# Optimization experiments

Hardware: AMD Instinct MI355X
Metric: run time of the kernel (lower is better)

Reference implementation:

```python
import jax, jax.numpy as jnp
import numpy as np

N = 4096        # nodes
E = 131072      # edges (avg degree 32)
IN_F = 256      # in_features
OUT_F = 64      # out_features per head
H = 8           # num_heads


def setup_inputs() -> dict:
    key = jax.random.key(0)
    k1, k2, k3, k4 = jax.random.split(key, 4)
    x = jax.random.normal(k1, (N, IN_F), dtype=jnp.float32)
    # xavier-ish scales for the learned params
    W = jax.random.normal(k2, (IN_F, OUT_F * H), dtype=jnp.float32) * 0.06
    a = jax.random.normal(k3, (2 * OUT_F, 1), dtype=jnp.float32) * 0.12
    edge_index = jax.random.randint(k4, (2, E), 0, N, dtype=jnp.int32)
    return {"x": x, "W": W, "a": a, "edge_index": edge_index}


def reference(x, W, a, edge_index):
    n = x.shape[0]
    Wh = (x @ W).reshape(n, H, OUT_F)          # [N, H, F]
    src, dst = edge_index[0], edge_index[1]
    # edge score: cat(Wh[src], Wh[dst]) @ a == Wh[src]@a1 + Wh[dst]@a2
    a1 = a[:OUT_F, 0]                           # [F]
    a2 = a[OUT_F:2 * OUT_F, 0]                  # [F]
    alpha_src = Wh @ a1                         # [N, H]
    alpha_dst = Wh @ a2                         # [N, H]
    edge_e = jax.nn.leaky_relu(alpha_src[src] + alpha_dst[dst], 0.2)  # [E, H]
    # dense scatter exactly as the original module (non-edges stay 0 in softmax)
    attention = jnp.zeros((n, n, H), dtype=x.dtype).at[src, dst].set(edge_e)
    attention = jax.nn.softmax(attention, axis=1)
    # dropout is identity in eval mode
    h_prime = jnp.einsum('nmh,mhf->nhf', attention, Wh)  # [N, H, F]
    return h_prime.reshape(n, H * OUT_F)        # concat=True
```

## Files before the change

### kernel.cpp

```cpp
#include <hip/hip_runtime.h>
#include <hip/hip_bf16.h>

constexpr int NN    = 4096;
constexpr int EE    = 131072;
constexpr int IN_F  = 256;
constexpr int OUT_F = 64;
constexpr int HH    = 8;
constexpr int HF    = OUT_F * HH;
constexpr int CAP   = 128;

typedef __attribute__((ext_vector_type(8))) short bf16x8;
typedef __attribute__((ext_vector_type(4))) float f32x4;

__device__ __forceinline__ unsigned short f2b(float f) {
    unsigned int u = __float_as_uint(f);
    u = u + 0x7FFFu + ((u >> 16) & 1u);
    return (unsigned short)(u >> 16);
}
__device__ __forceinline__ float b2f(unsigned int lo16) {
    return __uint_as_float(lo16 << 16);
}

__global__ __launch_bounds__(256) void prep(const float* __restrict__ W,
                                            unsigned short* __restrict__ WThi,
                                            unsigned short* __restrict__ WTlo,
                                            float* __restrict__ S,
                                            int* __restrict__ cnt) {
    int b = blockIdx.x, t = threadIdx.x;
    if (b < 64) {
        int n  = b * 8 + (t >> 5);
        int kb = (t & 31) * 8;
        unsigned short hi[8], lo[8];
#pragma unroll
        for (int j = 0; j < 8; ++j) {
            float f = W[(size_t)(kb + j) * HF + n];
            hi[j] = f2b(f);
            lo[j] = f2b(f - b2f(hi[j]));
        }
        size_t o = (size_t)n * 256 + kb;
        *(ushort4*)(WThi + o)     = make_ushort4(hi[0], hi[1], hi[2], hi[3]);
        *(ushort4*)(WThi + o + 4) = make_ushort4(hi[4], hi[5], hi[6], hi[7]);
        *(ushort4*)(WTlo + o)     = make_ushort4(lo[0], lo[1], lo[2], lo[3]);
        *(ushort4*)(WTlo + o + 4) = make_ushort4(lo[4], lo[5], lo[6], lo[7]);
    } else {
        int gt = (b - 64) * 256 + t;
        if (gt < NN) cnt[gt] = 0;
        else if (gt < NN + HF) S[gt - NN] = 0.f;
    }
}

__global__ __launch_bounds__(256) void gemm_mfma(const float* __restrict__ xf,
                                                 const unsigned short* __restrict__ WThi,
                                                 const unsigned short* __restrict__ WTlo,
                                                 const float* __restrict__ a,
                                                 const int* __restrict__ src,
                                                 const int* __restrict__ dst,
                                                 int* __restrict__ cnt,
                                                 int* __restrict__ csr_dst,
                                                 unsigned short* __restrict__ Whb,
                                                 float* __restrict__ asrc,
                                                 float* __restrict__ adst,
                                                 float* __restrict__ S) {
    __shared__ unsigned short Bhi_s[64][264];
    __shared__ unsigned short Blo_s[64][264];
    __shared__ float Scol[64];
    int b = blockIdx.x;
    int t = threadIdx.x;

    {
        int e = b * 256 + t;
        int s = src[e], d = dst[e];
        int pos = atomicAdd(&cnt[s], 1);
        csr_dst[(s << 7) + pos] = d;
    }

    int m0 = (b >> 3) * 64;
    int n0 = (b & 7) * 64;
    if (t < 64) Scol[t] = 0.f;

#pragma unroll
    for (int it = 0; it < 8; ++it) {
        int flat = it * 256 + t;
        int row  = flat >> 5;
        int cu   = flat & 31;
        *(uint4*)(&Bhi_s[row][cu * 8]) =
            *(const uint4*)(WThi + (size_t)(n0 + row) * 256 + cu * 8);
        *(uint4*)(&Blo_s[row][cu * 8]) =
            *(const uint4*)(WTlo + (size_t)(n0 + row) * 256 + cu * 8);
    }
    __syncthreads();

    int w  = t >> 6;
    int l  = t & 63;
    int kg = l >> 4;
    int ln = l & 15;
    int arow = m0 + w * 16 + ln;

    f32x4 acc[4] = {};

#pragma unroll
    for (int ks = 0; ks < 8; ++ks) {
        size_t aoff = (size_t)arow * 256 + ks * 32 + kg * 8;
        float4 v0 = *(const float4*)(xf + aoff);
        float4 v1 = *(const float4*)(xf + aoff + 4);
        float fv[8] = {v0.x, v0.y, v0.z, v0.w, v1.x, v1.y, v1.z, v1.w};
        bf16x8 ahi, alo;
#pragma unroll
        for (int j = 0; j < 8; ++j) {
            unsigned short hi = f2b(fv[j]);
            ahi[j] = (short)hi;
            alo[j] = (short)f2b(fv[j] - b2f(hi));
        }
#pragma unroll
        for (int nt = 0; nt < 4; ++nt) {
            bf16x8 bhi = *(const bf16x8*)(&Bhi_s[nt * 16 + ln][ks * 32 + kg * 8]);
            bf16x8 blo = *(const bf16x8*)(&Blo_s[nt * 16 + ln][ks * 32 + kg * 8]);
            acc[nt] = __builtin_amdgcn_mfma_f32_16x16x32_bf16(ahi, bhi, acc[nt], 0, 0, 0);
            acc[nt] = __builtin_amdgcn_mfma_f32_16x16x32_bf16(ahi, blo, acc[nt], 0, 0, 0);
            acc[nt] = __builtin_amdgcn_mfma_f32_16x16x32_bf16(alo, bhi, acc[nt], 0, 0, 0);
        }
    }

#pragma unroll
    for (int nt = 0; nt < 4; ++nt)
#pragma unroll
        for (int i = 0; i < 4; ++i) {
            int row = m0 + w * 16 + kg * 4 + i;
            Whb[(size_t)row * HF + n0 + nt * 16 + ln] = f2b(acc[nt][i]);
        }

    int h = n0 >> 6;
    float a1v[4], a2v[4];
#pragma unroll
    for (int nt = 0; nt < 4; ++nt) {
        a1v[nt] = a[nt * 16 + ln];
        a2v[nt] = a[OUT_F + nt * 16 + ln];
    }
#pragma unroll
    for (int i = 0; i < 4; ++i) {
        float p1 = acc[0][i] * a1v[0] + acc[1][i] * a1v[1] +
                   acc[2][i] * a1v[2] + acc[3][i] * a1v[3];
        float p2 = acc[0][i] * a2v[0] + acc[1][i] * a2v[1] +
                   acc[2][i] * a2v[2] + acc[3][i] * a2v[3];
#pragma unroll
        for (int mask = 1; mask < 16; mask <<= 1) {
            p1 += __shfl_xor(p1, mask);
            p2 += __shfl_xor(p2, mask);
        }
        if (ln == 0) {
            int node = m0 + w * 16 + kg * 4 + i;
            asrc[node * HH + h] = p1;
            adst[node * HH + h] = p2;
        }
    }

#pragma unroll
    for (int nt = 0; nt < 4; ++nt) {
        float cs = acc[nt][0] + acc[nt][1] + acc[nt][2] + acc[nt][3];
        cs += __shfl_xor(cs, 16);
        cs += __shfl_xor(cs, 32);
        if (kg == 0) atomicAdd(&Scol[nt * 16 + ln], cs);
    }
    __syncthreads();
    if (t < 64) atomicAdd(&S[n0 + t], Scol[t]);
}

__global__ __launch_bounds__(512) void aggregate_kernel(const unsigned short* __restrict__ Whb,
                                                        const float* __restrict__ asrc,
                                                        const float* __restrict__ adst,
                                                        const float* __restrict__ S,
                                                        const int* __restrict__ cnt,
                                                        const int* __restrict__ csr_dst,
                                                        float* __restrict__ out) {
    __shared__ int           midx[CAP];
    __shared__ unsigned char dupf[CAP];
    __shared__ float         wbuf[CAP * HH];
    __shared__ float         as_sh[HH];
    __shared__ float         denom[HH];
    __shared__ float         red[8][HF];
    int i = blockIdx.x;
    int t = threadIdx.x;
    int deg = cnt[i];
    if (deg > CAP) deg = CAP;

    if (t < HH) as_sh[t] = asrc[i * HH + t];
    for (int j = t; j < deg; j += 512) midx[j] = csr_dst[(i << 7) + j];
    __syncthreads();

    for (int j = t; j < deg; j += 512) {
        int m = midx[j];
        unsigned char f = 0;
        for (int k = 0; k < j; ++k)
            if (midx[k] == m) { f = 1; break; }
        dupf[j] = f;
    }
    __syncthreads();

    for (int idx = t; idx < deg * HH; idx += 512) {
        int sl = idx >> 3, h = idx & 7;
        float w = 0.f;
        if (!dupf[sl]) {
            float xv = as_sh[h] + adst[midx[sl] * HH + h];
            xv = (xv > 0.f) ? xv : 0.2f * xv;
            w = __expf(xv) - 1.f;
        }
        wbuf[idx] = w;
    }
    __syncthreads();

    if (t < 128) {
        int h = t >> 4, ln = t & 15;
        float p = 0.f;
        for (int sl = ln; sl < deg; sl += 16) p += wbuf[sl * HH + h];
#pragma unroll
        for (int mask = 1; mask < 16; mask <<= 1) p += __shfl_xor(p, mask);
        if (ln == 0) denom[h] = (float)NN + p;
    }
    __syncthreads();

    int g = t >> 6;
    int r = t & 63;
    int h = r >> 3;
    float accv[8] = {};

    int j0 = g, j1 = g + 8;
    uint4 u0 = {0, 0, 0, 0}, u1 = {0, 0, 0, 0};
    float w0 = 0.f, w1 = 0.f;
    if (j0 < deg) {
        w0 = wbuf[j0 * HH + h];
        u0 = *(const uint4*)(Whb + ((size_t)midx[j0] << 9) + (r << 3));
    }
    if (j1 < deg) {
        w1 = wbuf[j1 * HH + h];
        u1 = *(const uint4*)(Whb + ((size_t)midx[j1] << 9) + (r << 3));
    }
    int j = j0;
    while (j < deg) {
        int jn = j + 16;
        uint4 un = {0, 0, 0, 0};
        float wn = 0.f;
        if (jn < deg) {
            wn = wbuf[jn * HH + h];
            un = *(const uint4*)(Whb + ((size_t)midx[jn] << 9) + (r << 3));
        }
        accv[0] += w0 * b2f(u0.x & 0xFFFFu);
        accv[1] += w0 * b2f(u0.x >> 16);
        accv[2] += w0 * b2f(u0.y & 0xFFFFu);
        accv[3] += w0 * b2f(u0.y >> 16);
        accv[4] += w0 * b2f(u0.z & 0xFFFFu);
        accv[5] += w0 * b2f(u0.z >> 16);
        accv[6] += w0 * b2f(u0.w & 0xFFFFu);
        accv[7] += w0 * b2f(u0.w >> 16);
        u0 = u1; w0 = w1;
        u1 = un; w1 = wn;
        j += 8;
    }

    float4 v0 = {accv[0], accv[1], accv[2], accv[3]};
    float4 v1 = {accv[4], accv[5], accv[6], accv[7]};
    *(float4*)(&red[g][r * 8])     = v0;
    *(float4*)(&red[g][r * 8 + 4]) = v1;
    __syncthreads();

    float tot = S[t];
#pragma unroll
    for (int gg = 0; gg < 8; ++gg) tot += red[gg][t];
    out[((size_t)i << 9) + t] = tot / denom[t >> 6];
}

extern "C" void kernel_launch(void* const* d_in, const int* in_sizes, int n_in,
                              void* d_out, int out_size, void* d_ws, size_t ws_size,
                              hipStream_t stream) {
    const float* x  = (const float*)d_in[0];
    const float* W  = (const float*)d_in[1];
    const float* a  = (const float*)d_in[2];
    const int*   ei = (const int*)d_in[3];
    const int* src = ei;
    const int* dst = ei + EE;
    float* out = (float*)d_out;

    char* ws = (char*)d_ws;
    unsigned short* Whb  = (unsigned short*)(ws + 0);
    unsigned short* WThi = (unsigned short*)(ws + 4194304);
    unsigned short* WTlo = (unsigned short*)(ws + 4456448);
    float* asrc     = (float*)(ws + 4718592);
    float* adst     = (float*)(ws + 4849664);
    int*   csr_dst  = (int*)  (ws + 4980736);
    float* S        = (float*)(ws + 7077888);
    int*   cnt      = (int*)  (ws + 7079936);

    prep<<<82, 256, 0, stream>>>(W, WThi, WTlo, S, cnt);

    gemm_mfma<<<512, 256, 0, stream>>>(x, WThi, WTlo, a, src, dst,
                                       cnt, csr_dst, Whb, asrc, adst, S);

    aggregate_kernel<<<NN, 512, 0, stream>>>(Whb, asrc, adst, S, cnt, csr_dst, out);
}
```

Before: 118.3 us.

## Fuse W bf16 split into GEMM tile load and use bitmap dedup

```diff
diff --git a/kernel.cpp b/kernel.cpp
--- a/kernel.cpp
+++ b/kernel.cpp
@@ -21,37 +21,8 @@
     return __uint_as_float(lo16 << 16);
 }
 
-__global__ __launch_bounds__(256) void prep(const float* __restrict__ W,
-                                            unsigned short* __restrict__ WThi,
-                                            unsigned short* __restrict__ WTlo,
-                                            float* __restrict__ S,
-                                            int* __restrict__ cnt) {
-    int b = blockIdx.x, t = threadIdx.x;
-    if (b < 64) {
-        int n  = b * 8 + (t >> 5);
-        int kb = (t & 31) * 8;
-        unsigned short hi[8], lo[8];
-#pragma unroll
-        for (int j = 0; j < 8; ++j) {
-            float f = W[(size_t)(kb + j) * HF + n];
-            hi[j] = f2b(f);
-            lo[j] = f2b(f - b2f(hi[j]));
-        }
-        size_t o = (size_t)n * 256 + kb;
-        *(ushort4*)(WThi + o)     = make_ushort4(hi[0], hi[1], hi[2], hi[3]);
-        *(ushort4*)(WThi + o + 4) = make_ushort4(hi[4], hi[5], hi[6], hi[7]);
-        *(ushort4*)(WTlo + o)     = make_ushort4(lo[0], lo[1], lo[2], lo[3]);
-        *(ushort4*)(WTlo + o + 4) = make_ushort4(lo[4], lo[5], lo[6], lo[7]);
-    } else {
-        int gt = (b - 64) * 256 + t;
-        if (gt < NN) cnt[gt] = 0;
-        else if (gt < NN + HF) S[gt - NN] = 0.f;
-    }
-}
-
 __global__ __launch_bounds__(256) void gemm_mfma(const float* __restrict__ xf,
-                                                 const unsigned short* __restrict__ WThi,
-                                                 const unsigned short* __restrict__ WTlo,
+                                                 const float* __restrict__ Wf,
                                                  const float* __restrict__ a,
                                                  const int* __restrict__ src,
                                                  const int* __restrict__ dst,
@@ -78,15 +49,20 @@
     int n0 = (b & 7) * 64;
     if (t < 64) Scol[t] = 0.f;
 
-#pragma unroll
-    for (int it = 0; it < 8; ++it) {
+#pragma unroll 4
+    for (int it = 0; it < 16; ++it) {
         int flat = it * 256 + t;
-        int row  = flat >> 5;
-        int cu   = flat & 31;
-        *(uint4*)(&Bhi_s[row][cu * 8]) =
-            *(const uint4*)(WThi + (size_t)(n0 + row) * 256 + cu * 8);
-        *(uint4*)(&Blo_s[row][cu * 8]) =
-            *(const uint4*)(WTlo + (size_t)(n0 + row) * 256 + cu * 8);
+        int k    = flat >> 4;
+        int n4   = flat & 15;
+        float4 v = *(const float4*)(Wf + (size_t)k * HF + n0 + n4 * 4);
+        float fv[4] = {v.x, v.y, v.z, v.w};
+#pragma unroll
+        for (int j = 0; j < 4; ++j) {
+            unsigned short hi = f2b(fv[j]);
+            unsigned short lo = f2b(fv[j] - b2f(hi));
+            Bhi_s[n4 * 4 + j][k] = hi;
+            Blo_s[n4 * 4 + j][k] = lo;
+        }
     }
     __syncthreads();
 
@@ -174,6 +150,7 @@
                                                         float* __restrict__ out) {
     __shared__ int           midx[CAP];
     __shared__ unsigned char dupf[CAP];
+    __shared__ unsigned int  bmap[NN / 32];
     __shared__ float         wbuf[CAP * HH];
     __shared__ float         as_sh[HH];
     __shared__ float         denom[HH];
@@ -183,16 +160,15 @@
     int deg = cnt[i];
     if (deg > CAP) deg = CAP;
 
+    if (t < NN / 32) bmap[t] = 0u;
     if (t < HH) as_sh[t] = asrc[i * HH + t];
     for (int j = t; j < deg; j += 512) midx[j] = csr_dst[(i << 7) + j];
     __syncthreads();
 
     for (int j = t; j < deg; j += 512) {
         int m = midx[j];
-        unsigned char f = 0;
-        for (int k = 0; k < j; ++k)
-            if (midx[k] == m) { f = 1; break; }
-        dupf[j] = f;
+        unsigned int old = atomicOr(&bmap[m >> 5], 1u << (m & 31));
+        dupf[j] = (unsigned char)((old >> (m & 31)) & 1u);
     }
     __syncthreads();
 
@@ -280,18 +256,16 @@
     float* out = (float*)d_out;
 
     char* ws = (char*)d_ws;
-    unsigned short* Whb  = (unsigned short*)(ws + 0);
-    unsigned short* WThi = (unsigned short*)(ws + 4194304);
-    unsigned short* WTlo = (unsigned short*)(ws + 4456448);
-    float* asrc     = (float*)(ws + 4718592);
-    float* adst     = (float*)(ws + 4849664);
-    int*   csr_dst  = (int*)  (ws + 4980736);
-    float* S        = (float*)(ws + 7077888);
-    int*   cnt      = (int*)  (ws + 7079936);
-
-    prep<<<82, 256, 0, stream>>>(W, WThi, WTlo, S, cnt);
-
-    gemm_mfma<<<512, 256, 0, stream>>>(x, WThi, WTlo, a, src, dst,
+    unsigned short* Whb = (unsigned short*)(ws + 0);
+    float* asrc     = (float*)(ws + 4194304);
+    float* adst     = (float*)(ws + 4325376);
+    int*   csr_dst  = (int*)  (ws + 4456448);
+    float* S        = (float*)(ws + 6553600);
+    int*   cnt      = (int*)  (ws + 6555648);
+
+    hipMemsetAsync(ws + 6553600, 0, 2048 + 16384, stream);
+
+    gemm_mfma<<<512, 256, 0, stream>>>(x, W, a, src, dst,
                                        cnt, csr_dst, Whb, asrc, adst, S);
 
     aggregate_kernel<<<NN, 512, 0, stream>>>(Whb, asrc, adst, S, cnt, csr_dst, out);
```

Result: faster. 110.5 us (-6.6%).
